# Performance work log

Measured on AMD Instinct MI355X. Metric: run time of the kernel, lower is better.

The kernel has to match this reference:

```python
import jax, jax.numpy as jnp
import numpy as np

LN_EPS = 1e-5

def layer_norm(h, gamma, beta):
    mu = jnp.mean(h, axis=-1, keepdims=True)
    var = jnp.mean(jnp.square(h - mu), axis=-1, keepdims=True)
    return (h - mu) * jax.lax.rsqrt(var + LN_EPS) * gamma + beta

def gcn_conv(x, src, dst, W, b, n_nodes):
    # PyG GCNConv: h = X W; out = D^-1/2 (A + I) D^-1/2 h + b
    h = x @ W
    deg = jax.ops.segment_sum(jnp.ones_like(src, dtype=h.dtype), dst, num_segments=n_nodes)
    dinv = jax.lax.rsqrt(jnp.maximum(deg, 1.0))  # deg >= 1 due to self-loops
    norm = dinv[src] * dinv[dst]                  # [E]
    msg = h[src] * norm[:, None]                  # [E, d]
    return jax.ops.segment_sum(msg, dst, num_segments=n_nodes) + b

def setup_inputs() -> dict:
    key = jax.random.key(0)
    ks = jax.random.split(key, 8)
    N, E, Cin, Ch, Cout = 10000, 160000, 256, 512, 256
    x = jax.random.normal(ks[0], (N, Cin), dtype=jnp.float32)
    edge_index = jax.random.randint(ks[1], (2, E), 0, N, dtype=jnp.int64)
    W1 = jax.random.normal(ks[2], (Cin, Ch), dtype=jnp.float32) * (1.0 / np.sqrt(Cin))
    b1 = jnp.zeros((Ch,), dtype=jnp.float32)
    gamma1 = jnp.ones((Ch,), dtype=jnp.float32)
    beta1 = jnp.zeros((Ch,), dtype=jnp.float32)
    W2 = jax.random.normal(ks[3], (Ch, Cout), dtype=jnp.float32) * (1.0 / np.sqrt(Ch))
    b2 = jnp.zeros((Cout,), dtype=jnp.float32)
    gamma2 = jnp.ones((Cout,), dtype=jnp.float32)
    beta2 = jnp.zeros((Cout,), dtype=jnp.float32)
    return {"x": x, "edge_index": edge_index, "W1": W1, "b1": b1,
            "gamma1": gamma1, "beta1": beta1, "W2": W2, "b2": b2,
            "gamma2": gamma2, "beta2": beta2}

def reference(x, edge_index, W1, b1, gamma1, beta1, W2, b2, gamma2, beta2):
    n = x.shape[0]
    loops = jnp.arange(n, dtype=edge_index.dtype)
    src = jnp.concatenate([edge_index[0], loops])
    dst = jnp.concatenate([edge_index[1], loops])
    h = gcn_conv(x, src, dst, W1, b1, n)
    h = jax.nn.relu(layer_norm(h, gamma1, beta1))  # dropout = identity (eval mode)
    g = gcn_conv(h, src, dst, W2, b2, n)
    g = jax.nn.relu(layer_norm(g, gamma2, beta2))
    return g
```

## Files before the change

### kernel.cpp

```cpp
#include <hip/hip_runtime.h>
#include <hip/hip_bf16.h>


typedef __attribute__((ext_vector_type(8))) short bf16x8;
typedef __attribute__((ext_vector_type(4))) float f32x4;
typedef __attribute__((ext_vector_type(4))) unsigned short us4;
typedef __attribute__((ext_vector_type(8))) unsigned short us8;

template <int CW> struct VecT;
template <> struct VecT<4> { typedef us4 T; };
template <> struct VecT<8> { typedef us8 T; };

__device__ __forceinline__ unsigned short f2bf(float f) {
  unsigned int x = __float_as_uint(f);
  return (unsigned short)((x + 0x7FFFu + ((x >> 16) & 1u)) >> 16);
}
__device__ __forceinline__ float bf2f(unsigned short u) {
  return __uint_as_float((unsigned int)u << 16);
}

__device__ __forceinline__ void transpose_tile(const float* __restrict__ W,
                                               unsigned short* __restrict__ Wt,
                                               int K, int N, int n0, int k0,
                                               unsigned short (*t)[33], int tid) {
  int tx = tid & 31, ty = tid >> 5;
#pragma unroll
  for (int i = 0; i < 32; i += 8)
    t[ty + i][tx] = f2bf(W[(size_t)(k0 + ty + i) * N + n0 + tx]);
  __syncthreads();
#pragma unroll
  for (int i = 0; i < 32; i += 8)
    Wt[(size_t)(n0 + ty + i) * K + k0 + tx] = t[tx][ty + i];
  __syncthreads();
}

__global__ __launch_bounds__(256) void prep_kernel(
    const float* __restrict__ x, unsigned short* __restrict__ xb, long nelem,
    const int* __restrict__ dst, int E, int* __restrict__ deg,
    const float* __restrict__ W1, unsigned short* __restrict__ W1t,
    const float* __restrict__ W2, unsigned short* __restrict__ W2t,
    int Cin, int Ch, int Cout, int nbx, int nbe, int nbw1) {
  __shared__ unsigned short t[32][33];
  int bid = blockIdx.x, tid = threadIdx.x;
  if (bid < nbx) {
    long i = ((long)bid * 256 + tid) * 8;
    if (i + 8 <= nelem) {
      f32x4 a = *(const f32x4*)&x[i];
      f32x4 b = *(const f32x4*)&x[i + 4];
      us8 o;
      o[0] = f2bf(a.x); o[1] = f2bf(a.y); o[2] = f2bf(a.z); o[3] = f2bf(a.w);
      o[4] = f2bf(b.x); o[5] = f2bf(b.y); o[6] = f2bf(b.z); o[7] = f2bf(b.w);
      *(us8*)&xb[i] = o;
    }
  } else if (bid < nbx + nbe) {
    int e = (bid - nbx) * 256 + tid;
    if (e < E) atomicAdd(&deg[dst[e]], 1);
  } else if (bid < nbx + nbe + nbw1) {
    int ti = bid - nbx - nbe;
    int w = Ch >> 5;
    transpose_tile(W1, W1t, Cin, Ch, (ti % w) * 32, (ti / w) * 32, t, tid);
  } else {
    int ti = bid - nbx - nbe - nbw1;
    int w = Cout >> 5;
    transpose_tile(W2, W2t, Ch, Cout, (ti % w) * 32, (ti / w) * 32, t, tid);
  }
}

__global__ __launch_bounds__(1024) void scan_kernel(const int* __restrict__ deg, int N,
                                                    int* __restrict__ offsets,
                                                    int* __restrict__ curs,
                                                    float* __restrict__ dinv) {
  __shared__ int wsum[16];
  __shared__ int chunk_base;
  int tid = threadIdx.x;
  int lane = tid & 63, wid = tid >> 6;
  if (tid == 0) chunk_base = 0;
  __syncthreads();
  for (int c = 0; c < N; c += 1024) {
    int i = c + tid;
    int v = (i < N) ? deg[i] : 0;
    if (i < N) dinv[i] = rsqrtf((float)(v + 1));
    int s = v;
#pragma unroll
    for (int off = 1; off < 64; off <<= 1) {
      int t = __shfl_up(s, off, 64);
      if (lane >= off) s += t;
    }
    if (lane == 63) wsum[wid] = s;
    __syncthreads();
    if (wid == 0 && lane < 16) {
      int ws = wsum[lane];
      int t = ws;
#pragma unroll
      for (int off = 1; off < 16; off <<= 1) {
        int u = __shfl_up(t, off, 64);
        if (lane >= off) t += u;
      }
      wsum[lane] = t - ws;
    }
    __syncthreads();
    if (i < N) {
      int o = chunk_base + wsum[wid] + s - v;
      offsets[i] = o;
      curs[i] = o;
    }
    __syncthreads();
    if (tid == 1023) chunk_base += wsum[15] + s;
  }
  __syncthreads();
  if (tid == 0) offsets[N] = chunk_base;
}

__global__ __launch_bounds__(256) void fill_kernel(const int* __restrict__ src,
                                                   const int* __restrict__ dst, int E,
                                                   int* __restrict__ curs,
                                                   const float* __restrict__ dinv,
                                                   int2* __restrict__ csr_sn) {
  int e = blockIdx.x * 256 + threadIdx.x;
  if (e >= E) return;
  int s = src[e], d = dst[e];
  int p = atomicAdd(&curs[d], 1);
  csr_sn[p] = make_int2(s, __float_as_int(dinv[s] * dinv[d]));
}


template <int C, typename OutT>
__global__ __launch_bounds__(256) void agg_ln_kernel(
    const unsigned short* __restrict__ H, const int2* __restrict__ csr,
    const int* __restrict__ offs, const float* __restrict__ dinv,
    const float* __restrict__ bias, const float* __restrict__ gamma,
    const float* __restrict__ beta, OutT* __restrict__ out, int N) {
  constexpr int CW = C / 64;
  typedef typename VecT<CW>::T usv;
  int node = blockIdx.x * 4 + (threadIdx.x >> 6);
  if (node >= N) return;
  int lane = threadIdx.x & 63;
  int p0 = offs[node], p1 = offs[node + 1];
  int n = p1 - p0;
  float acc[CW] = {};
  auto fma_row = [&](usv hv, float wt) {
#pragma unroll
    for (int j = 0; j < CW; ++j) acc[j] = fmaf(bf2f(hv[j]), wt, acc[j]);
  };
  if (n > 0) {
    int2 e0 = csr[p0];
    usv h0 = *(const usv*)&H[(size_t)e0.x * C + lane * CW];
    if (n > 1) {
      int2 e1 = csr[p0 + 1];
      for (int p = p0; p + 2 < p1; ++p) {
        usv h1v = *(const usv*)&H[(size_t)e1.x * C + lane * CW];
        int2 e2 = csr[p + 2];
        fma_row(h0, __int_as_float(e0.y));
        e0 = e1; h0 = h1v; e1 = e2;
      }
      usv h1v = *(const usv*)&H[(size_t)e1.x * C + lane * CW];
      fma_row(h0, __int_as_float(e0.y));
      fma_row(h1v, __int_as_float(e1.y));
    } else {
      fma_row(h0, __int_as_float(e0.y));
    }
  }
  float dn = dinv[node];
  usv sv = *(const usv*)&H[(size_t)node * C + lane * CW];
  fma_row(sv, dn * dn);
#pragma unroll
  for (int j = 0; j < CW; ++j) acc[j] += bias[lane * CW + j];
  float s = 0.f, ss = 0.f;
#pragma unroll
  for (int j = 0; j < CW; ++j) { s += acc[j]; ss += acc[j] * acc[j]; }
#pragma unroll
  for (int off = 32; off > 0; off >>= 1) {
    s  += __shfl_xor(s, off, 64);
    ss += __shfl_xor(ss, off, 64);
  }
  float mu = s * (1.0f / C);
  float var = ss * (1.0f / C) - mu * mu;
  float r = rsqrtf(var + 1e-5f);
  float o[CW];
#pragma unroll
  for (int j = 0; j < CW; ++j)
    o[j] = fmaxf((acc[j] - mu) * r * gamma[lane * CW + j] + beta[lane * CW + j], 0.f);
  if constexpr (sizeof(OutT) == 4) {
#pragma unroll
    for (int j = 0; j < CW; ++j) out[(size_t)node * C + lane * CW + j] = o[j];
  } else {
    usv ov;
#pragma unroll
    for (int j = 0; j < CW; ++j) ov[j] = f2bf(o[j]);
    *(usv*)&out[(size_t)node * C + lane * CW] = ov;
  }
}


__global__ __launch_bounds__(256) void mfma_gemm_kernel(
    const unsigned short* __restrict__ A, const unsigned short* __restrict__ Bt,
    unsigned short* __restrict__ C, int M, int K, int N) {
  __shared__ unsigned short As[2][64 * 32];
  __shared__ unsigned short Bs[2][128 * 32];
  int tid = threadIdx.x;
  int lane = tid & 63, wid = tid >> 6;
  int bm = blockIdx.x * 64, bn = blockIdx.y * 128;
  int wm = (wid >> 1) * 32, wn = (wid & 1) * 64;
  int srow = tid >> 2;
  int schunk = tid & 3;
  int frow = lane & 15, fk = lane >> 4;
  f32x4 acc[2][4] = {};

  int scA = schunk ^ ((srow >> 1) & 3);
  int gaA = bm + srow; gaA = gaA < M ? gaA : M - 1;
  const unsigned short* gA0 = A + (size_t)gaA * K + scA * 8;
  int rowB0 = srow, rowB1 = 64 + srow;
  int scB0 = schunk ^ ((rowB0 >> 1) & 3);
  int scB1 = schunk ^ ((rowB1 >> 1) & 3);
  const unsigned short* gB0 = Bt + (size_t)(bn + rowB0) * K + scB0 * 8;
  const unsigned short* gB1 = Bt + (size_t)(bn + rowB1) * K + scB1 * 8;

  auto stage = [&](int k0, unsigned short* Ad, unsigned short* Bd) {
    __builtin_amdgcn_global_load_lds(
        (const __attribute__((address_space(1))) unsigned int*)(const void*)(gA0 + k0),
        (__attribute__((address_space(3))) unsigned int*)(void*)(Ad + (wid * 16) * 32),
        16, 0, 0);
    __builtin_amdgcn_global_load_lds(
        (const __attribute__((address_space(1))) unsigned int*)(const void*)(gB0 + k0),
        (__attribute__((address_space(3))) unsigned int*)(void*)(Bd + (wid * 16) * 32),
        16, 0, 0);
    __builtin_amdgcn_global_load_lds(
        (const __attribute__((address_space(1))) unsigned int*)(const void*)(gB1 + k0),
        (__attribute__((address_space(3))) unsigned int*)(void*)(Bd + (64 + wid * 16) * 32),
        16, 0, 0);
  };

  int nk = K >> 5;
  stage(0, As[0], Bs[0]);
  __syncthreads();
  for (int k = 0; k < nk; ++k) {
    unsigned short* Ac = As[k & 1];
    unsigned short* Bc = Bs[k & 1];
    if (k + 1 < nk) stage((k + 1) << 5, As[(k + 1) & 1], Bs[(k + 1) & 1]);
    bf16x8 af[2], bf[4];
#pragma unroll
    for (int mi = 0; mi < 2; ++mi) {
      int row = wm + mi * 16 + frow;
      int sc = fk ^ ((row >> 1) & 3);
      af[mi] = *(const bf16x8*)(Ac + row * 32 + sc * 8);
    }
#pragma unroll
    for (int ni = 0; ni < 4; ++ni) {
      int row = wn + ni * 16 + frow;
      int sc = fk ^ ((row >> 1) & 3);
      bf[ni] = *(const bf16x8*)(Bc + row * 32 + sc * 8);
    }
#pragma unroll
    for (int mi = 0; mi < 2; ++mi)
#pragma unroll
      for (int ni = 0; ni < 4; ++ni)
        acc[mi][ni] = __builtin_amdgcn_mfma_f32_16x16x32_bf16(af[mi], bf[ni], acc[mi][ni], 0, 0, 0);
    __syncthreads();
  }

  int row0 = bm + wm + fk * 4;
  int col0 = bn + wn + frow;
#pragma unroll
  for (int mi = 0; mi < 2; ++mi) {
#pragma unroll
    for (int ni = 0; ni < 4; ++ni) {
      int col = col0 + ni * 16;
#pragma unroll
      for (int r = 0; r < 4; ++r) {
        int row = row0 + mi * 16 + r;
        if (row < M) C[(size_t)row * N + col] = f2bf(acc[mi][ni][r]);
      }
    }
  }
}


extern "C" void kernel_launch(void* const* d_in, const int* in_sizes, int n_in,
                              void* d_out, int out_size, void* d_ws, size_t ws_size,
                              hipStream_t stream) {
  const float* x    = (const float*)d_in[0];
  const int*   ei   = (const int*)d_in[1];
  const float* W1   = (const float*)d_in[2];
  const float* b1   = (const float*)d_in[3];
  const float* ga1  = (const float*)d_in[4];
  const float* be1  = (const float*)d_in[5];
  const float* W2   = (const float*)d_in[6];
  const float* b2   = (const float*)d_in[7];
  const float* ga2  = (const float*)d_in[8];
  const float* be2  = (const float*)d_in[9];
  float* out = (float*)d_out;

  const int Ch   = in_sizes[3];
  const int Cout = in_sizes[7];
  const int Cin  = in_sizes[2] / Ch;
  const int N    = in_sizes[0] / Cin;
  const int E    = in_sizes[1] / 2;
  const int* srcp = ei;
  const int* dstp = ei + E;

  char* ws = (char*)d_ws;
  size_t off = 0;
  auto alloc = [&](size_t bytes) -> void* {
    off = (off + 255) & ~(size_t)255;
    void* p = ws + off;
    off += bytes;
    return p;
  };
  unsigned short* xb   = (unsigned short*)alloc((size_t)N * Cin * 2);
  unsigned short* h1w  = (unsigned short*)alloc((size_t)N * Ch * 2);
  unsigned short* h1b  = (unsigned short*)alloc((size_t)N * Ch * 2);
  unsigned short* h2w  = (unsigned short*)alloc((size_t)N * Cout * 2);
  unsigned short* W1t  = (unsigned short*)alloc((size_t)Cin * Ch * 2);
  unsigned short* W2t  = (unsigned short*)alloc((size_t)Ch * Cout * 2);
  int*   deg   = (int*)alloc((size_t)N * 4);
  int*   curs  = (int*)alloc((size_t)N * 4);
  int*   offs  = (int*)alloc((size_t)(N + 1) * 4);
  float* dinv  = (float*)alloc((size_t)N * 4);
  int2*  csr   = (int2*)alloc((size_t)E * 8);

  hipMemsetAsync(deg, 0, (size_t)N * 4, stream);

  long nelem = (long)N * Cin;
  int nbx  = (int)((nelem / 8 + 255) / 256);
  int nbe  = (E + 255) / 256;
  int nbw1 = (Cin / 32) * (Ch / 32);
  int nbw2 = (Ch / 32) * (Cout / 32);
  prep_kernel<<<nbx + nbe + nbw1 + nbw2, 256, 0, stream>>>(
      x, xb, nelem, dstp, E, deg, W1, W1t, W2, W2t, Cin, Ch, Cout, nbx, nbe, nbw1);
  scan_kernel<<<1, 1024, 0, stream>>>(deg, N, offs, curs, dinv);
  fill_kernel<<<nbe, 256, 0, stream>>>(srcp, dstp, E, curs, dinv, csr);

  mfma_gemm_kernel<<<dim3((N + 63) / 64, Ch / 128), 256, 0, stream>>>(
      xb, W1t, h1w, N, Cin, Ch);
  agg_ln_kernel<512, unsigned short><<<(N + 3) / 4, 256, 0, stream>>>(
      h1w, csr, offs, dinv, b1, ga1, be1, h1b, N);

  mfma_gemm_kernel<<<dim3((N + 63) / 64, Cout / 128), 256, 0, stream>>>(
      h1b, W2t, h2w, N, Ch, Cout);
  agg_ln_kernel<256, float><<<(N + 3) / 4, 256, 0, stream>>>(
      h2w, csr, offs, dinv, b2, ga2, be2, out, N);
}
```

Baseline: 182.1 us.

## Fuse whole GCN pipeline into persistent kernel with grid barriers

```diff
diff --git a/kernel.cpp b/kernel.cpp
--- a/kernel.cpp
+++ b/kernel.cpp
@@ -11,6 +11,10 @@
 template <> struct VecT<4> { typedef us4 T; };
 template <> struct VecT<8> { typedef us8 T; };
 
+#define GRID 512
+#define BLK 256
+#define CSRB 128
+
 __device__ __forceinline__ unsigned short f2bf(float f) {
   unsigned int x = __float_as_uint(f);
   return (unsigned short)((x + 0x7FFFu + ((x >> 16) & 1u)) >> 16);
@@ -18,6 +22,29 @@
 __device__ __forceinline__ float bf2f(unsigned short u) {
   return __uint_as_float((unsigned int)u << 16);
 }
+
+struct Params {
+  const float* x; const int* src; const int* dst;
+  const float* W1; const float* b1; const float* ga1; const float* be1;
+  const float* W2; const float* b2; const float* ga2; const float* be2;
+  float* out;
+  unsigned short* xb; unsigned short* h1w; unsigned short* h1b; unsigned short* h2w;
+  unsigned short* W1t; unsigned short* W2t;
+  int* deg; int* curs; int* offs; float* dinv; int2* csr; int* bsum; int* bar;
+  int N, E, Cin, Ch, Cout;
+};
+
+__device__ __forceinline__ void bar_sync(int* ctr, int target) {
+  __syncthreads();
+  if (threadIdx.x == 0) {
+    __threadfence();
+    atomicAdd(ctr, 1);
+    while (atomicAdd(ctr, 0) < target) __builtin_amdgcn_s_sleep(2);
+    __threadfence();
+  }
+  __syncthreads();
+}
+
 
 __device__ __forceinline__ void transpose_tile(const float* __restrict__ W,
                                                unsigned short* __restrict__ Wt,
@@ -34,172 +61,13 @@
   __syncthreads();
 }
 
-__global__ __launch_bounds__(256) void prep_kernel(
-    const float* __restrict__ x, unsigned short* __restrict__ xb, long nelem,
-    const int* __restrict__ dst, int E, int* __restrict__ deg,
-    const float* __restrict__ W1, unsigned short* __restrict__ W1t,
-    const float* __restrict__ W2, unsigned short* __restrict__ W2t,
-    int Cin, int Ch, int Cout, int nbx, int nbe, int nbw1) {
-  __shared__ unsigned short t[32][33];
-  int bid = blockIdx.x, tid = threadIdx.x;
-  if (bid < nbx) {
-    long i = ((long)bid * 256 + tid) * 8;
-    if (i + 8 <= nelem) {
-      f32x4 a = *(const f32x4*)&x[i];
-      f32x4 b = *(const f32x4*)&x[i + 4];
-      us8 o;
-      o[0] = f2bf(a.x); o[1] = f2bf(a.y); o[2] = f2bf(a.z); o[3] = f2bf(a.w);
-      o[4] = f2bf(b.x); o[5] = f2bf(b.y); o[6] = f2bf(b.z); o[7] = f2bf(b.w);
-      *(us8*)&xb[i] = o;
-    }
-  } else if (bid < nbx + nbe) {
-    int e = (bid - nbx) * 256 + tid;
-    if (e < E) atomicAdd(&deg[dst[e]], 1);
-  } else if (bid < nbx + nbe + nbw1) {
-    int ti = bid - nbx - nbe;
-    int w = Ch >> 5;
-    transpose_tile(W1, W1t, Cin, Ch, (ti % w) * 32, (ti / w) * 32, t, tid);
-  } else {
-    int ti = bid - nbx - nbe - nbw1;
-    int w = Cout >> 5;
-    transpose_tile(W2, W2t, Ch, Cout, (ti % w) * 32, (ti / w) * 32, t, tid);
-  }
-}
-
-__global__ __launch_bounds__(1024) void scan_kernel(const int* __restrict__ deg, int N,
-                                                    int* __restrict__ offsets,
-                                                    int* __restrict__ curs,
-                                                    float* __restrict__ dinv) {
-  __shared__ int wsum[16];
-  __shared__ int chunk_base;
-  int tid = threadIdx.x;
+__device__ __forceinline__ void gemm_tile(const unsigned short* __restrict__ A,
+                                          const unsigned short* __restrict__ Bt,
+                                          unsigned short* __restrict__ C,
+                                          int M, int K, int Nn, int bm, int bn,
+                                          unsigned short* As, unsigned short* Bs,
+                                          int tid) {
   int lane = tid & 63, wid = tid >> 6;
-  if (tid == 0) chunk_base = 0;
-  __syncthreads();
-  for (int c = 0; c < N; c += 1024) {
-    int i = c + tid;
-    int v = (i < N) ? deg[i] : 0;
-    if (i < N) dinv[i] = rsqrtf((float)(v + 1));
-    int s = v;
-#pragma unroll
-    for (int off = 1; off < 64; off <<= 1) {
-      int t = __shfl_up(s, off, 64);
-      if (lane >= off) s += t;
-    }
-    if (lane == 63) wsum[wid] = s;
-    __syncthreads();
-    if (wid == 0 && lane < 16) {
-      int ws = wsum[lane];
-      int t = ws;
-#pragma unroll
-      for (int off = 1; off < 16; off <<= 1) {
-        int u = __shfl_up(t, off, 64);
-        if (lane >= off) t += u;
-      }
-      wsum[lane] = t - ws;
-    }
-    __syncthreads();
-    if (i < N) {
-      int o = chunk_base + wsum[wid] + s - v;
-      offsets[i] = o;
-      curs[i] = o;
-    }
-    __syncthreads();
-    if (tid == 1023) chunk_base += wsum[15] + s;
-  }
-  __syncthreads();
-  if (tid == 0) offsets[N] = chunk_base;
-}
-
-__global__ __launch_bounds__(256) void fill_kernel(const int* __restrict__ src,
-                                                   const int* __restrict__ dst, int E,
-                                                   int* __restrict__ curs,
-                                                   const float* __restrict__ dinv,
-                                                   int2* __restrict__ csr_sn) {
-  int e = blockIdx.x * 256 + threadIdx.x;
-  if (e >= E) return;
-  int s = src[e], d = dst[e];
-  int p = atomicAdd(&curs[d], 1);
-  csr_sn[p] = make_int2(s, __float_as_int(dinv[s] * dinv[d]));
-}
-
-
-template <int C, typename OutT>
-__global__ __launch_bounds__(256) void agg_ln_kernel(
-    const unsigned short* __restrict__ H, const int2* __restrict__ csr,
-    const int* __restrict__ offs, const float* __restrict__ dinv,
-    const float* __restrict__ bias, const float* __restrict__ gamma,
-    const float* __restrict__ beta, OutT* __restrict__ out, int N) {
-  constexpr int CW = C / 64;
-  typedef typename VecT<CW>::T usv;
-  int node = blockIdx.x * 4 + (threadIdx.x >> 6);
-  if (node >= N) return;
-  int lane = threadIdx.x & 63;
-  int p0 = offs[node], p1 = offs[node + 1];
-  int n = p1 - p0;
-  float acc[CW] = {};
-  auto fma_row = [&](usv hv, float wt) {
-#pragma unroll
-    for (int j = 0; j < CW; ++j) acc[j] = fmaf(bf2f(hv[j]), wt, acc[j]);
-  };
-  if (n > 0) {
-    int2 e0 = csr[p0];
-    usv h0 = *(const usv*)&H[(size_t)e0.x * C + lane * CW];
-    if (n > 1) {
-      int2 e1 = csr[p0 + 1];
-      for (int p = p0; p + 2 < p1; ++p) {
-        usv h1v = *(const usv*)&H[(size_t)e1.x * C + lane * CW];
-        int2 e2 = csr[p + 2];
-        fma_row(h0, __int_as_float(e0.y));
-        e0 = e1; h0 = h1v; e1 = e2;
-      }
-      usv h1v = *(const usv*)&H[(size_t)e1.x * C + lane * CW];
-      fma_row(h0, __int_as_float(e0.y));
-      fma_row(h1v, __int_as_float(e1.y));
-    } else {
-      fma_row(h0, __int_as_float(e0.y));
-    }
-  }
-  float dn = dinv[node];
-  usv sv = *(const usv*)&H[(size_t)node * C + lane * CW];
-  fma_row(sv, dn * dn);
-#pragma unroll
-  for (int j = 0; j < CW; ++j) acc[j] += bias[lane * CW + j];
-  float s = 0.f, ss = 0.f;
-#pragma unroll
-  for (int j = 0; j < CW; ++j) { s += acc[j]; ss += acc[j] * acc[j]; }
-#pragma unroll
-  for (int off = 32; off > 0; off >>= 1) {
-    s  += __shfl_xor(s, off, 64);
-    ss += __shfl_xor(ss, off, 64);
-  }
-  float mu = s * (1.0f / C);
-  float var = ss * (1.0f / C) - mu * mu;
-  float r = rsqrtf(var + 1e-5f);
-  float o[CW];
-#pragma unroll
-  for (int j = 0; j < CW; ++j)
-    o[j] = fmaxf((acc[j] - mu) * r * gamma[lane * CW + j] + beta[lane * CW + j], 0.f);
-  if constexpr (sizeof(OutT) == 4) {
-#pragma unroll
-    for (int j = 0; j < CW; ++j) out[(size_t)node * C + lane * CW + j] = o[j];
-  } else {
-    usv ov;
-#pragma unroll
-    for (int j = 0; j < CW; ++j) ov[j] = f2bf(o[j]);
-    *(usv*)&out[(size_t)node * C + lane * CW] = ov;
-  }
-}
-
-
-__global__ __launch_bounds__(256) void mfma_gemm_kernel(
-    const unsigned short* __restrict__ A, const unsigned short* __restrict__ Bt,
-    unsigned short* __restrict__ C, int M, int K, int N) {
-  __shared__ unsigned short As[2][64 * 32];
-  __shared__ unsigned short Bs[2][128 * 32];
-  int tid = threadIdx.x;
-  int lane = tid & 63, wid = tid >> 6;
-  int bm = blockIdx.x * 64, bn = blockIdx.y * 128;
   int wm = (wid >> 1) * 32, wn = (wid & 1) * 64;
   int srow = tid >> 2;
   int schunk = tid & 3;
@@ -231,12 +99,13 @@
   };
 
   int nk = K >> 5;
-  stage(0, As[0], Bs[0]);
+  stage(0, As, Bs);
   __syncthreads();
   for (int k = 0; k < nk; ++k) {
-    unsigned short* Ac = As[k & 1];
-    unsigned short* Bc = Bs[k & 1];
-    if (k + 1 < nk) stage((k + 1) << 5, As[(k + 1) & 1], Bs[(k + 1) & 1]);
+    unsigned short* Ac = As + (k & 1) * 64 * 32;
+    unsigned short* Bc = Bs + (k & 1) * 128 * 32;
+    if (k + 1 < nk)
+      stage((k + 1) << 5, As + ((k + 1) & 1) * 64 * 32, Bs + ((k + 1) & 1) * 128 * 32);
     bf16x8 af[2], bf[4];
 #pragma unroll
     for (int mi = 0; mi < 2; ++mi) {
@@ -268,10 +137,183 @@
 #pragma unroll
       for (int r = 0; r < 4; ++r) {
         int row = row0 + mi * 16 + r;
-        if (row < M) C[(size_t)row * N + col] = f2bf(acc[mi][ni][r]);
-      }
-    }
-  }
+        if (row < M) C[(size_t)row * Nn + col] = f2bf(acc[mi][ni][r]);
+      }
+    }
+  }
+}
+
+template <int C, typename OutT>
+__device__ __forceinline__ void aggln_node(int node, int lane,
+                                           const unsigned short* __restrict__ H,
+                                           const int2* __restrict__ csr,
+                                           const int* __restrict__ offs,
+                                           const float* __restrict__ dinv,
+                                           const float* __restrict__ bias,
+                                           const float* __restrict__ gamma,
+                                           const float* __restrict__ beta,
+                                           OutT* __restrict__ out) {
+  constexpr int CW = C / 64;
+  typedef typename VecT<CW>::T usv;
+  int p0 = offs[node], p1 = offs[node + 1];
+  int n = p1 - p0;
+  float acc[CW] = {};
+  auto fma_row = [&](usv hv, float wt) {
+#pragma unroll
+    for (int j = 0; j < CW; ++j) acc[j] = fmaf(bf2f(hv[j]), wt, acc[j]);
+  };
+  if (n > 0) {
+    int2 e0 = csr[p0];
+    usv h0 = *(const usv*)&H[(size_t)e0.x * C + lane * CW];
+    if (n > 1) {
+      int2 e1 = csr[p0 + 1];
+      for (int p = p0; p + 2 < p1; ++p) {
+        usv h1v = *(const usv*)&H[(size_t)e1.x * C + lane * CW];
+        int2 e2 = csr[p + 2];
+        fma_row(h0, __int_as_float(e0.y));
+        e0 = e1; h0 = h1v; e1 = e2;
+      }
+      usv h1v = *(const usv*)&H[(size_t)e1.x * C + lane * CW];
+      fma_row(h0, __int_as_float(e0.y));
+      fma_row(h1v, __int_as_float(e1.y));
+    } else {
+      fma_row(h0, __int_as_float(e0.y));
+    }
+  }
+  float dn = dinv[node];
+  usv sv = *(const usv*)&H[(size_t)node * C + lane * CW];
+  fma_row(sv, dn * dn);
+#pragma unroll
+  for (int j = 0; j < CW; ++j) acc[j] += bias[lane * CW + j];
+  float s = 0.f, ss = 0.f;
+#pragma unroll
+  for (int j = 0; j < CW; ++j) { s += acc[j]; ss += acc[j] * acc[j]; }
+#pragma unroll
+  for (int off = 32; off > 0; off >>= 1) {
+    s  += __shfl_xor(s, off, 64);
+    ss += __shfl_xor(ss, off, 64);
+  }
+  float mu = s * (1.0f / C);
+  float var = ss * (1.0f / C) - mu * mu;
+  float r = rsqrtf(var + 1e-5f);
+  float o[CW];
+#pragma unroll
+  for (int j = 0; j < CW; ++j)
+    o[j] = fmaxf((acc[j] - mu) * r * gamma[lane * CW + j] + beta[lane * CW + j], 0.f);
+  if constexpr (sizeof(OutT) == 4) {
+#pragma unroll
+    for (int j = 0; j < CW; ++j) out[(size_t)node * C + lane * CW + j] = o[j];
+  } else {
+    usv ov;
+#pragma unroll
+    for (int j = 0; j < CW; ++j) ov[j] = f2bf(o[j]);
+    *(usv*)&out[(size_t)node * C + lane * CW] = ov;
+  }
+}
+
+
+__global__ __launch_bounds__(BLK, 2) void mega_kernel(Params p) {
+  __shared__ __align__(16) unsigned short As[2 * 64 * 32];
+  __shared__ __align__(16) unsigned short Bs[2 * 128 * 32];
+  const int bid = blockIdx.x, tid = threadIdx.x;
+  const int lane = tid & 63, wid = tid >> 6;
+  const int N = p.N, E = p.E, Cin = p.Cin, Ch = p.Ch, Cout = p.Cout;
+  const int nch = (N + 31) >> 5;
+
+  {
+    long nc8 = (long)N * Cin / 8;
+    for (long c = (long)bid * BLK + tid; c < nc8; c += (long)GRID * BLK) {
+      long i = c * 8;
+      f32x4 a = *(const f32x4*)&p.x[i];
+      f32x4 b = *(const f32x4*)&p.x[i + 4];
+      us8 o;
+      o[0] = f2bf(a.x); o[1] = f2bf(a.y); o[2] = f2bf(a.z); o[3] = f2bf(a.w);
+      o[4] = f2bf(b.x); o[5] = f2bf(b.y); o[6] = f2bf(b.z); o[7] = f2bf(b.w);
+      *(us8*)&p.xb[i] = o;
+    }
+    for (int e = bid * BLK + tid; e < E; e += GRID * BLK)
+      atomicAdd(&p.deg[p.dst[e]], 1);
+    int nbw1 = (Cin >> 5) * (Ch >> 5), nbw2 = (Ch >> 5) * (Cout >> 5);
+    unsigned short (*tt)[33] = (unsigned short(*)[33])As;
+    for (int ti = bid; ti < nbw1 + nbw2; ti += GRID) {
+      if (ti < nbw1) { int w = Ch >> 5; transpose_tile(p.W1, p.W1t, Cin, Ch, (ti % w) * 32, (ti / w) * 32, tt, tid); }
+      else { int t2 = ti - nbw1; int w = Cout >> 5; transpose_tile(p.W2, p.W2t, Ch, Cout, (t2 % w) * 32, (t2 / w) * 32, tt, tid); }
+    }
+  }
+  bar_sync(p.bar + 0, GRID);
+
+  if (bid < CSRB) {
+    for (int c = bid * 4 + wid; c < nch; c += CSRB * 4) {
+      if (lane < 32) {
+        int i = (c << 5) + lane;
+        int v = (i < N) ? p.deg[i] : 0;
+        if (i < N) p.dinv[i] = rsqrtf((float)(v + 1));
+        int s = v;
+#pragma unroll
+        for (int off = 1; off < 32; off <<= 1) {
+          int u = __shfl_up(s, off, 64);
+          if (lane >= off) s += u;
+        }
+        if (i < N) p.offs[i] = s - v;
+        if (lane == 31) p.bsum[c] = s;
+      }
+    }
+    bar_sync(p.bar + 1, CSRB);
+    if (bid == 0 && wid == 0) {
+      int base = 0;
+      for (int c0 = 0; c0 < nch; c0 += 64) {
+        int idx = c0 + lane;
+        int v = (idx < nch) ? p.bsum[idx] : 0;
+        int s = v;
+#pragma unroll
+        for (int off = 1; off < 64; off <<= 1) {
+          int u = __shfl_up(s, off, 64);
+          if (lane >= off) s += u;
+        }
+        if (idx < nch) p.bsum[idx] = base + s - v;
+        base += __shfl(s, 63, 64);
+      }
+      if (lane == 0) p.offs[N] = base;
+    }
+    bar_sync(p.bar + 2, CSRB);
+    for (int c = bid * 4 + wid; c < nch; c += CSRB * 4) {
+      if (lane < 32) {
+        int i = (c << 5) + lane;
+        if (i < N) {
+          int o = p.offs[i] + p.bsum[c];
+          p.offs[i] = o;
+          p.curs[i] = o;
+        }
+      }
+    }
+    bar_sync(p.bar + 3, CSRB);
+    for (int e = bid * BLK + tid; e < E; e += CSRB * BLK) {
+      int s = p.src[e], d = p.dst[e];
+      int pos = atomicAdd(&p.curs[d], 1);
+      p.csr[pos] = make_int2(s, __float_as_int(p.dinv[s] * p.dinv[d]));
+    }
+  } else {
+    int tm = (N + 63) >> 6, nt = tm * (Ch >> 7);
+    for (int t = bid - CSRB; t < nt; t += GRID - CSRB)
+      gemm_tile(p.xb, p.W1t, p.h1w, N, Cin, Ch, (t % tm) * 64, (t / tm) * 128, As, Bs, tid);
+  }
+  bar_sync(p.bar + 4, GRID);
+
+  for (int node = bid * 4 + wid; node < N; node += GRID * 4)
+    aggln_node<512, unsigned short>(node, lane, p.h1w, p.csr, p.offs, p.dinv,
+                                    p.b1, p.ga1, p.be1, p.h1b);
+  bar_sync(p.bar + 5, GRID);
+
+  {
+    int tm = (N + 63) >> 6, nt = tm * (Cout >> 7);
+    for (int t = bid; t < nt; t += GRID)
+      gemm_tile(p.h1b, p.W2t, p.h2w, N, Ch, Cout, (t % tm) * 64, (t / tm) * 128, As, Bs, tid);
+  }
+  bar_sync(p.bar + 6, GRID);
+
+  for (int node = bid * 4 + wid; node < N; node += GRID * 4)
+    aggln_node<256, float>(node, lane, p.h2w, p.csr, p.offs, p.dinv,
+                           p.b2, p.ga2, p.be2, p.out);
 }
 
 
@@ -297,6 +339,7 @@
   const int E    = in_sizes[1] / 2;
   const int* srcp = ei;
   const int* dstp = ei + E;
+  const int nch = (N + 31) >> 5;
 
   char* ws = (char*)d_ws;
   size_t off = 0;
@@ -312,31 +355,27 @@
   unsigned short* h2w  = (unsigned short*)alloc((size_t)N * Cout * 2);
   unsigned short* W1t  = (unsigned short*)alloc((size_t)Cin * Ch * 2);
   unsigned short* W2t  = (unsigned short*)alloc((size_t)Ch * Cout * 2);
-  int*   deg   = (int*)alloc((size_t)N * 4);
+  int*   degbar = (int*)alloc((size_t)(N + 32) * 4);
+  int*   deg = degbar;
+  int*   bar = degbar + N;
   int*   curs  = (int*)alloc((size_t)N * 4);
   int*   offs  = (int*)alloc((size_t)(N + 1) * 4);
   float* dinv  = (float*)alloc((size_t)N * 4);
   int2*  csr   = (int2*)alloc((size_t)E * 8);
-
-  hipMemsetAsync(deg, 0, (size_t)N * 4, stream);
-
-  long nelem = (long)N * Cin;
-  int nbx  = (int)((nelem / 8 + 255) / 256);
-  int nbe  = (E + 255) / 256;
-  int nbw1 = (Cin / 32) * (Ch / 32);
-  int nbw2 = (Ch / 32) * (Cout / 32);
-  prep_kernel<<<nbx + nbe + nbw1 + nbw2, 256, 0, stream>>>(
-      x, xb, nelem, dstp, E, deg, W1, W1t, W2, W2t, Cin, Ch, Cout, nbx, nbe, nbw1);
-  scan_kernel<<<1, 1024, 0, stream>>>(deg, N, offs, curs, dinv);
-  fill_kernel<<<nbe, 256, 0, stream>>>(srcp, dstp, E, curs, dinv, csr);
-
-  mfma_gemm_kernel<<<dim3((N + 63) / 64, Ch / 128), 256, 0, stream>>>(
-      xb, W1t, h1w, N, Cin, Ch);
-  agg_ln_kernel<512, unsigned short><<<(N + 3) / 4, 256, 0, stream>>>(
-      h1w, csr, offs, dinv, b1, ga1, be1, h1b, N);
-
-  mfma_gemm_kernel<<<dim3((N + 63) / 64, Cout / 128), 256, 0, stream>>>(
-      h1b, W2t, h2w, N, Ch, Cout);
-  agg_ln_kernel<256, float><<<(N + 3) / 4, 256, 0, stream>>>(
-      h2w, csr, offs, dinv, b2, ga2, be2, out, N);
-}
+  int*   bsum  = (int*)alloc((size_t)(nch + 1) * 4);
+
+  hipMemsetAsync(degbar, 0, (size_t)(N + 32) * 4, stream);
+
+  Params p;
+  p.x = x; p.src = srcp; p.dst = dstp;
+  p.W1 = W1; p.b1 = b1; p.ga1 = ga1; p.be1 = be1;
+  p.W2 = W2; p.b2 = b2; p.ga2 = ga2; p.be2 = be2;
+  p.out = out;
+  p.xb = xb; p.h1w = h1w; p.h1b = h1b; p.h2w = h2w;
+  p.W1t = W1t; p.W2t = W2t;
+  p.deg = deg; p.curs = curs; p.offs = offs; p.dinv = dinv;
+  p.csr = csr; p.bsum = bsum; p.bar = bar;
+  p.N = N; p.E = E; p.Cin = Cin; p.Ch = Ch; p.Cout = Cout;
+
+  mega_kernel<<<GRID, BLK, 0, stream>>>(p);
+}
```

Measured after the change: 465.2 us. 2.55x slower.
